# Performance work log

Hardware: AMD Instinct MI355X
Metric: run time of the kernel (lower is better)

The kernel has to match this reference:

```python
import jax, jax.numpy as jnp
import numpy as np

B_GRAPHS = 64
N_PER = 2048          # nodes per graph (uniform -> total = B*N)
D = 256               # hidden_dim
U = D // 2            # GRU units per direction
L_LAYERS = 2


def setup_inputs() -> dict:
    key = jax.random.key(0)
    ks = jax.random.split(key, 8)
    T = B_GRAPHS * N_PER
    states = jax.random.normal(ks[0], (T, D), dtype=jnp.float32)
    rng = np.random.default_rng(0)
    pos = np.zeros((B_GRAPHS, N_PER), dtype=np.int32)
    for g in range(B_GRAPHS):
        mask = rng.random(N_PER) < 0.5
        L = int(mask.sum())
        pos[g, mask] = rng.permutation(L).astype(np.int32) + 1
    node_positions = jnp.asarray(pos.reshape(-1))
    graph_sizes = jnp.full((B_GRAPHS,), N_PER, dtype=jnp.int32)
    # GRU params (Keras GRU reset_after=True): kernel [D,3u], recurrent [u,3u], bias [2,3u]
    def mk(k):
        k1, k2, k3 = jax.random.split(k, 3)
        K = jax.random.normal(k1, (L_LAYERS, D, 3 * U), dtype=jnp.float32) * 0.06
        R = jax.random.normal(k2, (L_LAYERS, U, 3 * U), dtype=jnp.float32) * 0.06
        b = jax.random.normal(k3, (L_LAYERS, 2, 3 * U), dtype=jnp.float32) * 0.02
        return K, R, b
    K_fwd, R_fwd, b_fwd = mk(ks[1])
    K_bwd, R_bwd, b_bwd = mk(ks[2])
    return {"states": states, "node_positions": node_positions,
            "graph_sizes": graph_sizes, "training": 0,
            "K_fwd": K_fwd, "R_fwd": R_fwd, "b_fwd": b_fwd,
            "K_bwd": K_bwd, "R_bwd": R_bwd, "b_bwd": b_bwd}


def _gru_dir(seq, mask, K, R, b, reverse):
    # seq [B,S,Din], mask [B,S] -> outputs [B,S,U] (Keras GRU, reset_after=True)
    xs = jnp.swapaxes(seq, 0, 1)                 # [S,B,Din]
    ms = jnp.swapaxes(mask, 0, 1)                # [S,B]
    x_proj = xs @ K + b[0]                       # [S,B,3U] input projections
    Bsz = seq.shape[0]
    h0 = jnp.zeros((Bsz, U), seq.dtype)
    def step(h, inp):
        xp, m = inp
        hp = h @ R + b[1]                        # [B,3U]
        xz, xr, xh = jnp.split(xp, 3, axis=-1)
        hz, hr, hh = jnp.split(hp, 3, axis=-1)
        z = jax.nn.sigmoid(xz + hz)
        r = jax.nn.sigmoid(xr + hr)
        cand = jnp.tanh(xh + r * hh)
        h_new = z * h + (1.0 - z) * cand
        h = jnp.where(m[:, None], h_new, h)      # padded steps carry state
        return h, h
    _, ys = jax.lax.scan(step, h0, (x_proj, ms), reverse=reverse)
    return jnp.swapaxes(ys, 0, 1)


def _forward(states, node_positions, graph_sizes, training,
             K_fwd, R_fwd, b_fwd, K_bwd, R_bwd, b_bwd):
    T = states.shape[0]
    B = graph_sizes.shape[0]
    S = T // B  # max leaf-seq length (uniform graph sizes; bounds leaf count)
    gid = jnp.repeat(jnp.arange(B, dtype=jnp.int32), graph_sizes,
                     total_repeat_length=T)                      # [T]
    leaf = node_positions != 0                                   # [T]
    pos0 = node_positions - 1                                    # valid where leaf
    slot = jnp.where(leaf, pos0, S)                              # dump non-leaves
    # Pack ragged leaf sequences into dense [B,S,D] (extra slot S = trash)
    seq = jnp.zeros((B, S + 1, D), states.dtype).at[gid, slot].set(states)[:, :S]
    smask = jnp.zeros((B, S + 1), bool).at[gid, slot].set(leaf)[:, :S]
    drop_rate = 0.1 * float(training)
    x = seq
    key = jax.random.key(42)
    for l in range(L_LAYERS):
        yf = _gru_dir(x, smask, K_fwd[l], R_fwd[l], b_fwd[l], reverse=False)
        yb = _gru_dir(x, smask, K_bwd[l], R_bwd[l], b_bwd[l], reverse=True)
        x = jnp.concatenate([yf, yb], axis=-1)                   # [B,S,D]
        if drop_rate > 0.0:
            key, sub = jax.random.split(key)
            keep = jax.random.bernoulli(sub, 1.0 - drop_rate, x.shape)
            x = jnp.where(keep, x / (1.0 - drop_rate), 0.0)
    # Unpack: leaf nodes get RNN output, non-leaves keep original state
    gathered = x[gid, jnp.clip(pos0, 0)]                         # [T,D]
    return jnp.where(leaf[:, None], gathered, states)


def reference(states, node_positions, graph_sizes, training,
              K_fwd, R_fwd, b_fwd, K_bwd, R_bwd, b_bwd):
    return _forward(states, node_positions, graph_sizes, training,
                    K_fwd, R_fwd, b_fwd, K_bwd, R_bwd, b_bwd)
```

## Files before the change

kernel.cpp:

```cpp
#include <hip/hip_runtime.h>
#include <hip/hip_bf16.h>

#define B_GRAPHS 64
#define NPER     2048
#define T_NODES  (B_GRAPHS*NPER)
#define D_DIM    256
#define U_DIM    128
#define TU       384
#define XPW      768

typedef unsigned short ushortT;
typedef unsigned int   uint32;

typedef __attribute__((ext_vector_type(4))) float  f32x4;
typedef __attribute__((ext_vector_type(8))) __bf16 bf16x8;
typedef _Float16 f16;
typedef __attribute__((ext_vector_type(2))) _Float16 f16x2;

#define GAS __attribute__((address_space(1)))
#define LOG2E_F 1.4426950408889634f

static __device__ __forceinline__ ushortT f2bf(float f) {
  union { float f; uint32 u; } a; a.f = f;
  uint32 u = a.u;
  return (ushortT)((u + 0x7fffu + ((u >> 16) & 1u)) >> 16);
}
static __device__ __forceinline__ float bf2f(ushortT h) {
  union { uint32 u; float f; } a; a.u = ((uint32)h) << 16; return a.f;
}
static __device__ __forceinline__ f16x2 u2h(uint32 u) {
  union { uint32 u; f16x2 h; } x; x.u = u; return x.h;
}
static __device__ __forceinline__ float dot2f(f16x2 a, f16x2 b, float c) {
#if __has_builtin(__builtin_amdgcn_fdot2)
  return __builtin_amdgcn_fdot2(a, b, c, false);
#else
  return c + (float)a.x * (float)b.x + (float)a.y * (float)b.y;
#endif
}
static __device__ __forceinline__ float rcpf(float x) {
#if __has_builtin(__builtin_amdgcn_rcpf)
  return __builtin_amdgcn_rcpf(x);
#else
  return 1.0f / x;
#endif
}
static __device__ __forceinline__ float exp2f_hw(float x) {
#if __has_builtin(__builtin_amdgcn_exp2f)
  return __builtin_amdgcn_exp2f(x);
#else
  return __expf(0.69314718055994531f * x);
#endif
}
static __device__ __forceinline__ ushortT gload_u16(const ushortT* p) {
  return *(const GAS ushortT*)p;
}
static __device__ __forceinline__ void gstore_u16(ushortT* p, ushortT v) {
  *(GAS ushortT*)p = v;
}

static __device__ __forceinline__ float xor32_sum(float v) {
  return v + __shfl_xor(v, 32);
}

__global__ __launch_bounds__(256) void prep_kernel(
    const float* __restrict__ Kf, const float* __restrict__ Kb,
    const float* __restrict__ bfw, const float* __restrict__ bbw,
    ushortT* __restrict__ Wt, float* __restrict__ b0)
{
  int idx = blockIdx.x * 256 + threadIdx.x;
  if (idx < 2 * XPW * D_DIM) {
    int l = idx / (XPW * D_DIM);
    int rem = idx % (XPW * D_DIM);
    int c = rem / D_DIM, k = rem % D_DIM;
    float v = (c < TU) ? Kf[(size_t)l * D_DIM * TU + (size_t)k * TU + c]
                       : Kb[(size_t)l * D_DIM * TU + (size_t)k * TU + (c - TU)];
    float sc = ((c % TU) < 256) ? LOG2E_F : 2.0f * LOG2E_F;
    Wt[idx] = f2bf(v * sc);
  } else {
    int i2 = idx - 2 * XPW * D_DIM;
    if (i2 < 2 * XPW) {
      int l = i2 / XPW, c = i2 % XPW;
      float v = (c < TU) ? bfw[l * 2 * TU + c] : bbw[l * 2 * TU + (c - TU)];
      float sc = ((c % TU) < 256) ? LOG2E_F : 2.0f * LOG2E_F;
      b0[i2] = v * sc;
    }
  }
}

__global__ __launch_bounds__(256) void nodeofL_kernel(
    const int* __restrict__ pos, int* __restrict__ nodeof, int* __restrict__ L)
{
  int g = blockIdx.x, tid = threadIdx.x;
  __shared__ int red[256];
  int cnt = 0;
  for (int i = 0; i < NPER / 256; ++i) {
    int t = g * NPER + i * 256 + tid;
    int p = pos[t];
    if (p) { nodeof[g * NPER + p - 1] = t; cnt++; }
  }
  red[tid] = cnt; __syncthreads();
  for (int s = 128; s > 0; s >>= 1) {
    if (tid < s) red[tid] += red[tid + s];
    __syncthreads();
  }
  if (tid == 0) L[g] = red[0];
}

#if __has_builtin(__builtin_amdgcn_global_load_lds)
#define GLD_LDS(gsrc, ldst) \
  __builtin_amdgcn_global_load_lds((const GAS void*)(gsrc), \
                                   (__attribute__((address_space(3))) void*)(ldst), 16, 0, 0)
#define HAVE_GLD_LDS 1
#else
#define HAVE_GLD_LDS 0
#endif

__global__ __launch_bounds__(256) void gemm_kernel(
    const float* __restrict__ statesA, const ushortT* __restrict__ Adense,
    const ushortT* __restrict__ Wt, const float* __restrict__ b0,
    const int* __restrict__ nodeof, const int* __restrict__ L,
    ushortT* __restrict__ xp, int layer, int mode)
{
  int mblk = blockIdx.x, nblk = blockIdx.y;
  int g = mblk >> 4;
  int sBase = (mblk & 15) << 7;
  int Lg = L[g];
  if (sBase >= Lg) return;

  __shared__ __align__(16) ushortT As[128 * 32];
  __shared__ __align__(16) ushortT Bs[128 * 32];

  int tid = threadIdx.x;
  int lane = tid & 63, wid = tid >> 6;
  int wr = wid >> 1, wc = wid & 1;
  f32x4 acc[4][4];
  for (int i = 0; i < 4; i++) for (int n = 0; n < 4; n++) acc[i][n] = (f32x4){0.f,0.f,0.f,0.f};

  for (int kb = 0; kb < 8; ++kb) {
    __syncthreads();
    for (int c = 0; c < 2; ++c) {
      int flat = c * 4096 + tid * 16;
      int col = flat >> 6;
      size_t srcB = ((size_t)(layer * XPW + nblk * 128 + col)) * 512 + kb * 64 + (flat & 63);
#if HAVE_GLD_LDS
      GLD_LDS((const char*)Wt + srcB, (char*)Bs + c * 4096 + wid * 1024);
#else
      *(uint4*)((char*)Bs + flat) = *(const uint4*)((const char*)Wt + srcB);
#endif
    }
    if (mode) {
      for (int c = 0; c < 2; ++c) {
        int flat = c * 4096 + tid * 16;
        int row = flat >> 6;
        size_t srcA = ((size_t)(mblk * 128 + row)) * 512 + kb * 64 + (flat & 63);
#if HAVE_GLD_LDS
        GLD_LDS((const char*)Adense + srcA, (char*)As + c * 4096 + wid * 1024);
#else
        *(uint4*)((char*)As + flat) = *(const uint4*)((const char*)Adense + srcA);
#endif
      }
    } else {
      for (int c = 0; c < 2; ++c) {
        int flat = c * 4096 + tid * 16;
        int row = flat >> 6;
        int s = sBase + row;
        if (s < Lg) {
          int nt = nodeof[g * NPER + s];
          const float* sp = statesA + (size_t)nt * D_DIM + kb * 32 + ((flat & 63) >> 1);
          float4 u0 = *(const float4*)sp;
          float4 u1 = *(const float4*)(sp + 4);
          union { ushortT us[8]; uint4 v; } pk;
          pk.us[0] = f2bf(u0.x); pk.us[1] = f2bf(u0.y); pk.us[2] = f2bf(u0.z); pk.us[3] = f2bf(u0.w);
          pk.us[4] = f2bf(u1.x); pk.us[5] = f2bf(u1.y); pk.us[6] = f2bf(u1.z); pk.us[7] = f2bf(u1.w);
          *(uint4*)((char*)As + flat) = pk.v;
        }
      }
    }
    __syncthreads();

    bf16x8 af[4], bfr[4];
    for (int i = 0; i < 4; i++) {
      int off = (wr * 64 + i * 16 + (lane & 15)) * 32 + (lane >> 4) * 8;
      af[i] = *(const bf16x8*)&As[off];
    }
    for (int n = 0; n < 4; n++) {
      int off = (wc * 64 + n * 16 + (lane & 15)) * 32 + (lane >> 4) * 8;
      bfr[n] = *(const bf16x8*)&Bs[off];
    }
    for (int i = 0; i < 4; i++)
      for (int n = 0; n < 4; n++)
        acc[i][n] = __builtin_amdgcn_mfma_f32_16x16x32_bf16(af[i], bfr[n], acc[i][n], 0, 0, 0);
  }

  for (int n = 0; n < 4; n++) {
    int gcol = nblk * 128 + wc * 64 + n * 16 + (lane & 15);
    float bb = b0[layer * XPW + gcol];
    for (int i = 0; i < 4; i++) {
      int rowBase = mblk * 128 + wr * 64 + i * 16 + (lane >> 4) * 4;
      for (int v = 0; v < 4; v++)
        xp[(size_t)(rowBase + v) * XPW + gcol] = f2bf(acc[i][n][v] + bb);
    }
  }
}

__global__ __launch_bounds__(256) void rec_kernel(
    const ushortT* __restrict__ xp,
    const float* __restrict__ Rf, const float* __restrict__ Rb,
    const float* __restrict__ bfw, const float* __restrict__ bbw,
    const int* __restrict__ L, ushortT* __restrict__ y, int layer)
{
  int g = blockIdx.x, dir = blockIdx.y;
  int Lg = L[g];
  if (Lg == 0) return;
  int tid = threadIdx.x;
  int wave = tid >> 6, lane = tid & 63;
  int jl = lane & 31, half = lane >> 5;
  int j = wave * 32 + jl;

  __shared__ __align__(16) f16 hpk[2][128];

  const float* R  = (dir ? Rb : Rf) + (size_t)layer * U_DIM * TU;
  const float* b1 = (dir ? bbw : bfw) + layer * 2 * TU + TU;

  f16x2 rz[32], rg[32], rh[32];
  #pragma unroll
  for (int m = 0; m < 32; ++m) {
    int k = half * 64 + 2 * m;
    const float* p0 = R + (size_t)k * TU;
    const float* p1 = p0 + TU;
    f16x2 a, b, c;
    a.x = (f16)(p0[j] * LOG2E_F);                a.y = (f16)(p1[j] * LOG2E_F);
    b.x = (f16)(p0[128 + j] * LOG2E_F);          b.y = (f16)(p1[128 + j] * LOG2E_F);
    c.x = (f16)(p0[256 + j] * (2.0f * LOG2E_F)); c.y = (f16)(p1[256 + j] * (2.0f * LOG2E_F));
    rz[m] = a; rg[m] = b; rh[m] = c;
  }
  float bz = half ? 0.0f : b1[j] * LOG2E_F;
  float br = half ? 0.0f : b1[128 + j] * LOG2E_F;
  float bh = half ? 0.0f : b1[256 + j] * (2.0f * LOG2E_F);

  if (tid < 128) hpk[0][tid] = (f16)0.0f;
  float hreg = 0.0f;
  __syncthreads();

  size_t xbase = (size_t)g * NPER * XPW + (size_t)dir * TU;
  int pos0 = dir ? (Lg - 1) : 0;
  const int xstep = dir ? -XPW : XPW;
  const int ystep = dir ? -D_DIM : D_DIM;
  const ushortT* xnext = xp + xbase + (size_t)pos0 * XPW;
  ushortT* ynext = y + ((size_t)(g * NPER + pos0)) * D_DIM + dir * U_DIM + j;

  ushortT xz0=0,xr0=0,xh0=0, xz1=0,xr1=0,xh1=0, xz2=0,xr2=0,xh2=0, xz3=0,xr3=0,xh3=0;
  { xz0 = gload_u16(xnext+j); xr0 = gload_u16(xnext+128+j); xh0 = gload_u16(xnext+256+j); }
  xnext += xstep;
  if (1 < Lg) { xz1 = gload_u16(xnext+j); xr1 = gload_u16(xnext+128+j); xh1 = gload_u16(xnext+256+j); }
  xnext += xstep;
  if (2 < Lg) { xz2 = gload_u16(xnext+j); xr2 = gload_u16(xnext+128+j); xh2 = gload_u16(xnext+256+j); }
  xnext += xstep;
  if (3 < Lg) { xz3 = gload_u16(xnext+j); xr3 = gload_u16(xnext+128+j); xh3 = gload_u16(xnext+256+j); }
  xnext += xstep;

#define GRU_STEP(P, XZ, XR, XH, SS)                                              \
  {                                                                              \
    const int s_ = (SS);                                                         \
    float xzf = bf2f(XZ), xrf = bf2f(XR), xhf = bf2f(XH);                        \
    if (s_ + 4 < Lg) {                                                           \
      XZ = gload_u16(xnext + j);                                                 \
      XR = gload_u16(xnext + 128 + j);                                           \
      XH = gload_u16(xnext + 256 + j);                                           \
    }                                                                            \
    xnext += xstep;                                                              \
    const uint4* hv = (const uint4*)&hpk[P][half * 64];                          \
    uint32 hw[32];                                                               \
    _Pragma("unroll")                                                            \
    for (int q8 = 0; q8 < 8; ++q8) {                                             \
      uint4 v_ = hv[q8];                                                         \
      hw[4*q8] = v_.x; hw[4*q8+1] = v_.y; hw[4*q8+2] = v_.z; hw[4*q8+3] = v_.w;  \
    }                                                                            \
    float az0 = bz, ar0 = br, ah0 = bh, az1 = 0.f, ar1 = 0.f, ah1 = 0.f;         \
    _Pragma("unroll")                                                            \
    for (int m = 0; m < 32; m += 2) {                                            \
      az0 = dot2f(u2h(hw[m]),   rz[m],   az0);                                   \
      ar0 = dot2f(u2h(hw[m]),   rg[m],   ar0);                                   \
      ah0 = dot2f(u2h(hw[m]),   rh[m],   ah0);                                   \
      az1 = dot2f(u2h(hw[m+1]), rz[m+1], az1);                                   \
      ar1 = dot2f(u2h(hw[m+1]), rg[m+1], ar1);                                   \
      ah1 = dot2f(u2h(hw[m+1]), rh[m+1], ah1);                                   \
    }                                                                            \
    float hz = xor32_sum(az0 + az1);                                             \
    float hr = xor32_sum(ar0 + ar1);                                             \
    float hh = xor32_sum(ah0 + ah1);                                             \
    float z = rcpf(1.0f + exp2f_hw(-(xzf + hz)));                                \
    float r = rcpf(1.0f + exp2f_hw(-(xrf + hr)));                                \
    float a = xhf + r * hh;                                                      \
    float e = exp2f_hw(__builtin_fabsf(a));                                      \
    float th = 1.0f - 2.0f * rcpf(e + 1.0f);                                     \
    float cand = __builtin_copysignf(th, a);                                     \
    float hnew = cand + z * (hreg - cand);                                       \
    hreg = hnew;                                                                 \
    if (half) {                                                                  \
      gstore_u16(ynext, f2bf(hnew));                                             \
    } else {                                                                     \
      hpk[(P) ^ 1][j] = (f16)hnew;                                               \
    }                                                                            \
    ynext += ystep;                                                              \
    asm volatile("s_waitcnt lgkmcnt(0)" ::: "memory");                           \
    __builtin_amdgcn_sched_barrier(0);                                           \
    __builtin_amdgcn_s_barrier();                                                \
    __builtin_amdgcn_sched_barrier(0);                                           \
  }

  for (int s = 0; s < Lg; s += 4) {
    GRU_STEP(0, xz0, xr0, xh0, s);
    if (s + 1 < Lg) GRU_STEP(1, xz1, xr1, xh1, s + 1);
    if (s + 2 < Lg) GRU_STEP(0, xz2, xr2, xh2, s + 2);
    if (s + 3 < Lg) GRU_STEP(1, xz3, xr3, xh3, s + 3);
  }
#undef GRU_STEP
}

__global__ __launch_bounds__(256) void unpack_kernel(
    const float* __restrict__ states, const int* __restrict__ pos,
    const ushortT* __restrict__ y, float* __restrict__ out)
{
  int node = blockIdx.x * 4 + (threadIdx.x >> 6);
  int lane = threadIdx.x & 63;
  int p = pos[node];
  int g = node >> 11;
  float4 v;
  if (p) {
    const ushortT* yp = y + (size_t)(g * NPER + p - 1) * D_DIM + lane * 4;
    v = make_float4(bf2f(yp[0]), bf2f(yp[1]), bf2f(yp[2]), bf2f(yp[3]));
  } else {
    v = *(const float4*)(states + (size_t)node * D_DIM + lane * 4);
  }
  *(float4*)(out + (size_t)node * D_DIM + lane * 4) = v;
}

extern "C" void kernel_launch(void* const* d_in, const int* in_sizes, int n_in,
                              void* d_out, int out_size, void* d_ws, size_t ws_size,
                              hipStream_t stream) {
  const float* states = (const float*)d_in[0];
  const int*   pos    = (const int*)d_in[1];
  const float* Kf  = (const float*)d_in[4];
  const float* Rf  = (const float*)d_in[5];
  const float* bfw = (const float*)d_in[6];
  const float* Kb  = (const float*)d_in[7];
  const float* Rb  = (const float*)d_in[8];
  const float* bbw = (const float*)d_in[9];

  char* ws = (char*)d_ws;
  int*     L      = (int*)(ws + 0);
  int*     nodeof = (int*)(ws + 256);
  ushortT* Wt     = (ushortT*)(ws + 524544);
  float*   b0     = (float*)(ws + 1310976);
  ushortT* xp     = (ushortT*)(ws + 1317120);
  ushortT* y      = (ushortT*)(ws + 202643712);

  prep_kernel<<<1542, 256, 0, stream>>>(Kf, Kb, bfw, bbw, Wt, b0);
  nodeofL_kernel<<<64, 256, 0, stream>>>(pos, nodeof, L);

  dim3 ggrid(1024, 6);
  dim3 rgrid(64, 2);

  gemm_kernel<<<ggrid, 256, 0, stream>>>(states, (const ushortT*)nullptr, Wt, b0, nodeof, L, xp, 0, 0);
  rec_kernel<<<rgrid, 256, 0, stream>>>(xp, Rf, Rb, bfw, bbw, L, y, 0);
  gemm_kernel<<<ggrid, 256, 0, stream>>>(states, y, Wt, b0, nodeof, L, xp, 1, 1);
  rec_kernel<<<rgrid, 256, 0, stream>>>(xp, Rf, Rb, bfw, bbw, L, y, 1);

  unpack_kernel<<<32768, 256, 0, stream>>>(states, pos, y, (float*)d_out);
}
```

Baseline: 1.240 ms.

## Compute GRU recurrent matvec with MFMA 16x16x32 instead of fdot2

The recurrent h@R product in the sequential GRU kernel moves from per-lane packed fp16 dot2 instructions with a cross-half shuffle reduction onto MFMA 16x16x32 f16 instructions. The hidden state is broadcast as the A operand, so only row 0 of each output tile is used. Each lane now handles two hidden units and R is held in registers as B fragments. This aims to shorten the per-step latency on the serial critical path, but spends most of the MFMA work on redundant rows and adds chained MFMA latency in every step.

```diff
diff --git a/kernel.cpp b/kernel.cpp
--- a/kernel.cpp
+++ b/kernel.cpp
@@ -15,7 +15,7 @@
 typedef __attribute__((ext_vector_type(4))) float  f32x4;
 typedef __attribute__((ext_vector_type(8))) __bf16 bf16x8;
 typedef _Float16 f16;
-typedef __attribute__((ext_vector_type(2))) _Float16 f16x2;
+typedef __attribute__((ext_vector_type(8))) _Float16 f16x8;
 
 #define GAS __attribute__((address_space(1)))
 #define LOG2E_F 1.4426950408889634f
@@ -28,16 +28,6 @@
 static __device__ __forceinline__ float bf2f(ushortT h) {
   union { uint32 u; float f; } a; a.u = ((uint32)h) << 16; return a.f;
 }
-static __device__ __forceinline__ f16x2 u2h(uint32 u) {
-  union { uint32 u; f16x2 h; } x; x.u = u; return x.h;
-}
-static __device__ __forceinline__ float dot2f(f16x2 a, f16x2 b, float c) {
-#if __has_builtin(__builtin_amdgcn_fdot2)
-  return __builtin_amdgcn_fdot2(a, b, c, false);
-#else
-  return c + (float)a.x * (float)b.x + (float)a.y * (float)b.y;
-#endif
-}
 static __device__ __forceinline__ float rcpf(float x) {
 #if __has_builtin(__builtin_amdgcn_rcpf)
   return __builtin_amdgcn_rcpf(x);
@@ -57,10 +47,6 @@
 }
 static __device__ __forceinline__ void gstore_u16(ushortT* p, ushortT v) {
   *(GAS ushortT*)p = v;
-}
-
-static __device__ __forceinline__ float xor32_sum(float v) {
-  return v + __shfl_xor(v, 32);
 }
 
 __global__ __launch_bounds__(256) void prep_kernel(
@@ -215,32 +201,38 @@
   if (Lg == 0) return;
   int tid = threadIdx.x;
   int wave = tid >> 6, lane = tid & 63;
-  int jl = lane & 31, half = lane >> 5;
-  int j = wave * 32 + jl;
+  int l2 = lane & 15;
+  int j0 = wave * 32;
+  int u0 = j0 + l2, u1 = j0 + 16 + l2;
 
   __shared__ __align__(16) f16 hpk[2][128];
 
-  const float* R  = (dir ? Rb : Rf) + (size_t)layer * U_DIM * TU;
-  const float* b1 = (dir ? bbw : bfw) + layer * 2 * TU + TU;
-
-  f16x2 rz[32], rg[32], rh[32];
+  const float* Rsrc = (dir ? Rb : Rf) + (size_t)layer * U_DIM * TU;
+  const float* b1p  = (dir ? bbw : bfw) + layer * 2 * TU + TU;
+
+  f16x8 bw[6][4];
   #pragma unroll
-  for (int m = 0; m < 32; ++m) {
-    int k = half * 64 + 2 * m;
-    const float* p0 = R + (size_t)k * TU;
-    const float* p1 = p0 + TU;
-    f16x2 a, b, c;
-    a.x = (f16)(p0[j] * LOG2E_F);                a.y = (f16)(p1[j] * LOG2E_F);
-    b.x = (f16)(p0[128 + j] * LOG2E_F);          b.y = (f16)(p1[128 + j] * LOG2E_F);
-    c.x = (f16)(p0[256 + j] * (2.0f * LOG2E_F)); c.y = (f16)(p1[256 + j] * (2.0f * LOG2E_F));
-    rz[m] = a; rg[m] = b; rh[m] = c;
-  }
-  float bz = half ? 0.0f : b1[j] * LOG2E_F;
-  float br = half ? 0.0f : b1[128 + j] * LOG2E_F;
-  float bh = half ? 0.0f : b1[256 + j] * (2.0f * LOG2E_F);
+  for (int t = 0; t < 6; ++t) {
+    int gate = t >> 1;
+    float sc = (gate < 2) ? LOG2E_F : 2.0f * LOG2E_F;
+    int col = gate * 128 + j0 + (t & 1) * 16 + l2;
+    #pragma unroll
+    for (int q = 0; q < 4; ++q) {
+      union { f16 h[8]; f16x8 v; } pk;
+      #pragma unroll
+      for (int e = 0; e < 8; ++e) {
+        int k = q * 32 + (lane >> 4) * 8 + e;
+        pk.h[e] = (f16)(Rsrc[(size_t)k * TU + col] * sc);
+      }
+      bw[t][q] = pk.v;
+    }
+  }
+  float bz0 = b1p[u0] * LOG2E_F,                bz1 = b1p[u1] * LOG2E_F;
+  float br0 = b1p[128 + u0] * LOG2E_F,          br1 = b1p[128 + u1] * LOG2E_F;
+  float bh0 = b1p[256 + u0] * (2.0f * LOG2E_F), bh1 = b1p[256 + u1] * (2.0f * LOG2E_F);
 
   if (tid < 128) hpk[0][tid] = (f16)0.0f;
-  float hreg = 0.0f;
+  float hreg0 = 0.0f, hreg1 = 0.0f;
   __syncthreads();
 
   size_t xbase = (size_t)g * NPER * XPW + (size_t)dir * TU;
@@ -248,60 +240,85 @@
   const int xstep = dir ? -XPW : XPW;
   const int ystep = dir ? -D_DIM : D_DIM;
   const ushortT* xnext = xp + xbase + (size_t)pos0 * XPW;
-  ushortT* ynext = y + ((size_t)(g * NPER + pos0)) * D_DIM + dir * U_DIM + j;
-
-  ushortT xz0=0,xr0=0,xh0=0, xz1=0,xr1=0,xh1=0, xz2=0,xr2=0,xh2=0, xz3=0,xr3=0,xh3=0;
-  { xz0 = gload_u16(xnext+j); xr0 = gload_u16(xnext+128+j); xh0 = gload_u16(xnext+256+j); }
+  ushortT* ynext = y + ((size_t)(g * NPER + pos0)) * D_DIM + dir * U_DIM;
+
+#define LOADX(S0,S1,S2,S3,S4,S5, COND)                                           \
+  if (COND) {                                                                    \
+    S0 = gload_u16(xnext + u0);       S1 = gload_u16(xnext + u1);                \
+    S2 = gload_u16(xnext + 128 + u0); S3 = gload_u16(xnext + 128 + u1);          \
+    S4 = gload_u16(xnext + 256 + u0); S5 = gload_u16(xnext + 256 + u1);          \
+  }                                                                              \
   xnext += xstep;
-  if (1 < Lg) { xz1 = gload_u16(xnext+j); xr1 = gload_u16(xnext+128+j); xh1 = gload_u16(xnext+256+j); }
-  xnext += xstep;
-  if (2 < Lg) { xz2 = gload_u16(xnext+j); xr2 = gload_u16(xnext+128+j); xh2 = gload_u16(xnext+256+j); }
-  xnext += xstep;
-  if (3 < Lg) { xz3 = gload_u16(xnext+j); xr3 = gload_u16(xnext+128+j); xh3 = gload_u16(xnext+256+j); }
-  xnext += xstep;
-
-#define GRU_STEP(P, XZ, XR, XH, SS)                                              \
+
+  ushortT Xa0=0,Xa1=0,Xa2=0,Xa3=0,Xa4=0,Xa5=0;
+  ushortT Xb0=0,Xb1=0,Xb2=0,Xb3=0,Xb4=0,Xb5=0;
+  ushortT Xc0=0,Xc1=0,Xc2=0,Xc3=0,Xc4=0,Xc5=0;
+  ushortT Xd0=0,Xd1=0,Xd2=0,Xd3=0,Xd4=0,Xd5=0;
+  LOADX(Xa0,Xa1,Xa2,Xa3,Xa4,Xa5, true)
+  LOADX(Xb0,Xb1,Xb2,Xb3,Xb4,Xb5, 1 < Lg)
+  LOADX(Xc0,Xc1,Xc2,Xc3,Xc4,Xc5, 2 < Lg)
+  LOADX(Xd0,Xd1,Xd2,Xd3,Xd4,Xd5, 3 < Lg)
+
+#define MFMA_F16 __builtin_amdgcn_mfma_f32_16x16x32_f16
+
+#define GRU_STEP(P, X0,X1,X2,X3,X4,X5, SS)                                       \
   {                                                                              \
     const int s_ = (SS);                                                         \
-    float xzf = bf2f(XZ), xrf = bf2f(XR), xhf = bf2f(XH);                        \
-    if (s_ + 4 < Lg) {                                                           \
-      XZ = gload_u16(xnext + j);                                                 \
-      XR = gload_u16(xnext + 128 + j);                                           \
-      XH = gload_u16(xnext + 256 + j);                                           \
-    }                                                                            \
-    xnext += xstep;                                                              \
-    const uint4* hv = (const uint4*)&hpk[P][half * 64];                          \
-    uint32 hw[32];                                                               \
-    _Pragma("unroll")                                                            \
-    for (int q8 = 0; q8 < 8; ++q8) {                                             \
-      uint4 v_ = hv[q8];                                                         \
-      hw[4*q8] = v_.x; hw[4*q8+1] = v_.y; hw[4*q8+2] = v_.z; hw[4*q8+3] = v_.w;  \
-    }                                                                            \
-    float az0 = bz, ar0 = br, ah0 = bh, az1 = 0.f, ar1 = 0.f, ah1 = 0.f;         \
-    _Pragma("unroll")                                                            \
-    for (int m = 0; m < 32; m += 2) {                                            \
-      az0 = dot2f(u2h(hw[m]),   rz[m],   az0);                                   \
-      ar0 = dot2f(u2h(hw[m]),   rg[m],   ar0);                                   \
-      ah0 = dot2f(u2h(hw[m]),   rh[m],   ah0);                                   \
-      az1 = dot2f(u2h(hw[m+1]), rz[m+1], az1);                                   \
-      ar1 = dot2f(u2h(hw[m+1]), rg[m+1], ar1);                                   \
-      ah1 = dot2f(u2h(hw[m+1]), rh[m+1], ah1);                                   \
-    }                                                                            \
-    float hz = xor32_sum(az0 + az1);                                             \
-    float hr = xor32_sum(ar0 + ar1);                                             \
-    float hh = xor32_sum(ah0 + ah1);                                             \
-    float z = rcpf(1.0f + exp2f_hw(-(xzf + hz)));                                \
-    float r = rcpf(1.0f + exp2f_hw(-(xrf + hr)));                                \
-    float a = xhf + r * hh;                                                      \
-    float e = exp2f_hw(__builtin_fabsf(a));                                      \
-    float th = 1.0f - 2.0f * rcpf(e + 1.0f);                                     \
-    float cand = __builtin_copysignf(th, a);                                     \
-    float hnew = cand + z * (hreg - cand);                                       \
-    hreg = hnew;                                                                 \
-    if (half) {                                                                  \
-      gstore_u16(ynext, f2bf(hnew));                                             \
-    } else {                                                                     \
-      hpk[(P) ^ 1][j] = (f16)hnew;                                               \
+      \
+    const char* hb = (const char*)&hpk[P][0] + ((lane >> 4) * 16);               \
+    f16x8 a0 = *(const f16x8*)(hb);                                              \
+    f16x8 a1 = *(const f16x8*)(hb + 64);                                         \
+    f16x8 a2 = *(const f16x8*)(hb + 128);                                        \
+    f16x8 a3 = *(const f16x8*)(hb + 192);                                        \
+    float xz0f = bf2f(X0), xz1f = bf2f(X1);                                      \
+    float xr0f = bf2f(X2), xr1f = bf2f(X3);                                      \
+    float xh0f = bf2f(X4), xh1f = bf2f(X5);                                      \
+    LOADX(X0,X1,X2,X3,X4,X5, s_ + 4 < Lg)                                        \
+    const f32x4 zv = {0.f, 0.f, 0.f, 0.f};                                       \
+    f32x4 t0 = MFMA_F16(a0, bw[0][0], zv, 0, 0, 0);                              \
+    f32x4 t1 = MFMA_F16(a0, bw[1][0], zv, 0, 0, 0);                              \
+    f32x4 t2 = MFMA_F16(a0, bw[2][0], zv, 0, 0, 0);                              \
+    f32x4 t3 = MFMA_F16(a0, bw[3][0], zv, 0, 0, 0);                              \
+    f32x4 t4 = MFMA_F16(a0, bw[4][0], zv, 0, 0, 0);                              \
+    f32x4 t5 = MFMA_F16(a0, bw[5][0], zv, 0, 0, 0);                              \
+    t0 = MFMA_F16(a1, bw[0][1], t0, 0, 0, 0);                                    \
+    t1 = MFMA_F16(a1, bw[1][1], t1, 0, 0, 0);                                    \
+    t2 = MFMA_F16(a1, bw[2][1], t2, 0, 0, 0);                                    \
+    t3 = MFMA_F16(a1, bw[3][1], t3, 0, 0, 0);                                    \
+    t4 = MFMA_F16(a1, bw[4][1], t4, 0, 0, 0);                                    \
+    t5 = MFMA_F16(a1, bw[5][1], t5, 0, 0, 0);                                    \
+    t0 = MFMA_F16(a2, bw[0][2], t0, 0, 0, 0);                                    \
+    t1 = MFMA_F16(a2, bw[1][2], t1, 0, 0, 0);                                    \
+    t2 = MFMA_F16(a2, bw[2][2], t2, 0, 0, 0);                                    \
+    t3 = MFMA_F16(a2, bw[3][2], t3, 0, 0, 0);                                    \
+    t4 = MFMA_F16(a2, bw[4][2], t4, 0, 0, 0);                                    \
+    t5 = MFMA_F16(a2, bw[5][2], t5, 0, 0, 0);                                    \
+    t0 = MFMA_F16(a3, bw[0][3], t0, 0, 0, 0);                                    \
+    t1 = MFMA_F16(a3, bw[1][3], t1, 0, 0, 0);                                    \
+    t2 = MFMA_F16(a3, bw[2][3], t2, 0, 0, 0);                                    \
+    t3 = MFMA_F16(a3, bw[3][3], t3, 0, 0, 0);                                    \
+    t4 = MFMA_F16(a3, bw[4][3], t4, 0, 0, 0);                                    \
+    t5 = MFMA_F16(a3, bw[5][3], t5, 0, 0, 0);                                    \
+                     \
+    float z0 = rcpf(1.0f + exp2f_hw(-(xz0f + t0[0] + bz0)));                     \
+    float z1 = rcpf(1.0f + exp2f_hw(-(xz1f + t1[0] + bz1)));                     \
+    float r0 = rcpf(1.0f + exp2f_hw(-(xr0f + t2[0] + br0)));                     \
+    float r1 = rcpf(1.0f + exp2f_hw(-(xr1f + t3[0] + br1)));                     \
+    float a0v = xh0f + r0 * (t4[0] + bh0);                                       \
+    float a1v = xh1f + r1 * (t5[0] + bh1);                                       \
+    float e0 = exp2f_hw(__builtin_fabsf(a0v));                                   \
+    float e1 = exp2f_hw(__builtin_fabsf(a1v));                                   \
+    float th0 = 1.0f - 2.0f * rcpf(e0 + 1.0f);                                   \
+    float th1 = 1.0f - 2.0f * rcpf(e1 + 1.0f);                                   \
+    float c0 = __builtin_copysignf(th0, a0v);                                    \
+    float c1 = __builtin_copysignf(th1, a1v);                                    \
+    float hn0 = c0 + z0 * (hreg0 - c0); hreg0 = hn0;                             \
+    float hn1 = c1 + z1 * (hreg1 - c1); hreg1 = hn1;                             \
+    if (lane < 16) {                                                             \
+      gstore_u16(ynext + u0, f2bf(hn0));                                         \
+      gstore_u16(ynext + u1, f2bf(hn1));                                         \
+      hpk[(P) ^ 1][u0] = (f16)hn0;                                               \
+      hpk[(P) ^ 1][u1] = (f16)hn1;                                               \
     }                                                                            \
     ynext += ystep;                                                              \
     asm volatile("s_waitcnt lgkmcnt(0)" ::: "memory");                           \
@@ -311,12 +328,14 @@
   }
 
   for (int s = 0; s < Lg; s += 4) {
-    GRU_STEP(0, xz0, xr0, xh0, s);
-    if (s + 1 < Lg) GRU_STEP(1, xz1, xr1, xh1, s + 1);
-    if (s + 2 < Lg) GRU_STEP(0, xz2, xr2, xh2, s + 2);
-    if (s + 3 < Lg) GRU_STEP(1, xz3, xr3, xh3, s + 3);
+    GRU_STEP(0, Xa0,Xa1,Xa2,Xa3,Xa4,Xa5, s);
+    if (s + 1 < Lg) GRU_STEP(1, Xb0,Xb1,Xb2,Xb3,Xb4,Xb5, s + 1);
+    if (s + 2 < Lg) GRU_STEP(0, Xc0,Xc1,Xc2,Xc3,Xc4,Xc5, s + 2);
+    if (s + 3 < Lg) GRU_STEP(1, Xd0,Xd1,Xd2,Xd3,Xd4,Xd5, s + 3);
   }
 #undef GRU_STEP
+#undef MFMA_F16
+#undef LOADX
 }
 
 __global__ __launch_bounds__(256) void unpack_kernel(
```

Measured after the change: 1.369 ms. 1.1x slower.

## Overlap non-leaf state copy with layer-0 recurrence on idle CUs

Applied to the files above, without the earlier changes.

Extra blocks are added to the first recurrent kernel launch to copy non-leaf node states into the output while the latency-bound GRU recurrence runs on only 128 blocks. The final unpack kernel now writes only leaf nodes. The aim is to hide memory-bound copy traffic behind the serial recurrence. The copy blocks may compete for bandwidth or CU resources with the recurrence blocks.

```diff
diff --git a/kernel.cpp b/kernel.cpp
--- a/kernel.cpp
+++ b/kernel.cpp
@@ -8,6 +8,7 @@
 #define U_DIM    128
 #define TU       384
 #define XPW      768
+#define NCB      128
 
 typedef unsigned short ushortT;
 typedef unsigned int   uint32;
@@ -204,12 +205,27 @@
   }
 }
 
+template <int COPY>
 __global__ __launch_bounds__(256) void rec_kernel(
     const ushortT* __restrict__ xp,
     const float* __restrict__ Rf, const float* __restrict__ Rb,
     const float* __restrict__ bfw, const float* __restrict__ bbw,
-    const int* __restrict__ L, ushortT* __restrict__ y, int layer)
-{
+    const int* __restrict__ L, ushortT* __restrict__ y, int layer,
+    const float* __restrict__ states, const int* __restrict__ pos,
+    float* __restrict__ outp)
+{
+  if (COPY && blockIdx.x >= B_GRAPHS) {
+    int cb = (blockIdx.x - B_GRAPHS) + (blockIdx.y ? NCB : 0);
+    int lane = threadIdx.x & 63;
+    for (int node = cb * 4 + (threadIdx.x >> 6); node < T_NODES; node += 2 * NCB * 4) {
+      if (pos[node] == 0) {
+        float4 v = *(const float4*)(states + (size_t)node * D_DIM + lane * 4);
+        *(float4*)(outp + (size_t)node * D_DIM + lane * 4) = v;
+      }
+    }
+    return;
+  }
+
   int g = blockIdx.x, dir = blockIdx.y;
   int Lg = L[g];
   if (Lg == 0) return;
@@ -320,20 +336,16 @@
 }
 
 __global__ __launch_bounds__(256) void unpack_kernel(
-    const float* __restrict__ states, const int* __restrict__ pos,
-    const ushortT* __restrict__ y, float* __restrict__ out)
+    const int* __restrict__ pos, const ushortT* __restrict__ y,
+    float* __restrict__ out)
 {
   int node = blockIdx.x * 4 + (threadIdx.x >> 6);
   int lane = threadIdx.x & 63;
   int p = pos[node];
+  if (!p) return;
   int g = node >> 11;
-  float4 v;
-  if (p) {
-    const ushortT* yp = y + (size_t)(g * NPER + p - 1) * D_DIM + lane * 4;
-    v = make_float4(bf2f(yp[0]), bf2f(yp[1]), bf2f(yp[2]), bf2f(yp[3]));
-  } else {
-    v = *(const float4*)(states + (size_t)node * D_DIM + lane * 4);
-  }
+  const ushortT* yp = y + (size_t)(g * NPER + p - 1) * D_DIM + lane * 4;
+  float4 v = make_float4(bf2f(yp[0]), bf2f(yp[1]), bf2f(yp[2]), bf2f(yp[3]));
   *(float4*)(out + (size_t)node * D_DIM + lane * 4) = v;
 }
 
@@ -361,12 +373,13 @@
   nodeofL_kernel<<<64, 256, 0, stream>>>(pos, nodeof, L);
 
   dim3 ggrid(1024, 6);
-  dim3 rgrid(64, 2);
+  dim3 rgrid0(B_GRAPHS + NCB, 2);
+  dim3 rgrid1(B_GRAPHS, 2);
 
   gemm_kernel<<<ggrid, 256, 0, stream>>>(states, (const ushortT*)nullptr, Wt, b0, nodeof, L, xp, 0, 0);
-  rec_kernel<<<rgrid, 256, 0, stream>>>(xp, Rf, Rb, bfw, bbw, L, y, 0);
+  rec_kernel<1><<<rgrid0, 256, 0, stream>>>(xp, Rf, Rb, bfw, bbw, L, y, 0, states, pos, (float*)d_out);
   gemm_kernel<<<ggrid, 256, 0, stream>>>(states, y, Wt, b0, nodeof, L, xp, 1, 1);
-  rec_kernel<<<rgrid, 256, 0, stream>>>(xp, Rf, Rb, bfw, bbw, L, y, 1);
-
-  unpack_kernel<<<32768, 256, 0, stream>>>(states, pos, y, (float*)d_out);
-}
+  rec_kernel<0><<<rgrid1, 256, 0, stream>>>(xp, Rf, Rb, bfw, bbw, L, y, 1, states, pos, (float*)d_out);
+
+  unpack_kernel<<<32768, 256, 0, stream>>>(pos, y, (float*)d_out);
+}
```

After: 1.230 ms. About the same (-0.8%).
